# Optimization experiments

Measured on AMD Instinct MI355X. Metric: run time of the kernel, lower is better.

## Reference

```python
import jax, jax.numpy as jnp
import numpy as np

NEG = -1000000000.0  # mask fill value from the original code


def setup_inputs() -> dict:
    key = jax.random.key(0)
    k1, k2, k3 = jax.random.split(key, 3)
    B, L, H, E = 2, 2048, 16, 64
    S, D = L, E
    queries = jax.random.normal(k1, (B, L, H, E), dtype=jnp.float32)
    keys = jax.random.normal(k2, (B, S, H, E), dtype=jnp.float32)
    values = jax.random.normal(k3, (B, S, H, D), dtype=jnp.float32)
    return {"queries": queries, "keys": keys, "values": values}


def reference(queries, keys, values):
    B, L, H, E = queries.shape
    S = keys.shape[1]
    scale = 1.0 / np.sqrt(E)
    # scores: [B, H, L, S]
    scores = jnp.einsum('blhe,bshe->bhls', queries, keys)
    # Faithful to original: tf.where(band_part(ones,-1,0), -1e9, scores)
    # i.e. fill -1e9 where the LOWER triangle (incl. diagonal) is True.
    tril = jnp.tril(jnp.ones((L, S), dtype=bool))  # [L, S]
    scores = jnp.where(tril[None, None, :, :], jnp.float32(NEG), scores)
    # scale applied AFTER masking, as in the original
    A = jax.nn.softmax(scale * scores, axis=-1)
    # dropout is identity at inference
    V = jnp.einsum('bhls,bshd->blhd', A, values)
    return V
```

## Files before the change

### kernel.cpp

```cpp
#include <hip/hip_runtime.h>


#define B_ 2
#define L_ 2048
#define H_ 16
#define E_ 64
#define S_ 2048
#define D_ 64
#define QSCALE 0.18033688011112042f

typedef __attribute__((ext_vector_type(4))) float f32x4;
typedef __attribute__((ext_vector_type(16))) float f32x16;
typedef __attribute__((ext_vector_type(8))) short short8;
typedef __attribute__((ext_vector_type(2))) unsigned int uint2v;
typedef __attribute__((ext_vector_type(4))) unsigned int uint4v;
typedef unsigned short ushort;

__device__ __forceinline__ unsigned short f2bf(float f) {
  unsigned int u = __builtin_bit_cast(unsigned int, f);
  u = (u + 0x7FFFu + ((u >> 16) & 1u)) >> 16;
  return (unsigned short)u;
}
__device__ __forceinline__ unsigned int pkbf(float a, float b) {
  return (unsigned int)f2bf(a) | ((unsigned int)f2bf(b) << 16);
}
__device__ __forceinline__ unsigned cvtpk(float a, float b) {
  unsigned r;
  asm("v_cvt_pk_bf16_f32 %0, %1, %2" : "=v"(r) : "v"(a), "v"(b));
  return r;
}
__device__ __forceinline__ uint2v plswap(unsigned a, unsigned b, int hi) {
#if __has_builtin(__builtin_amdgcn_permlane32_swap)
  (void)hi;
  return __builtin_amdgcn_permlane32_swap(a, b, false, false);
#else
  unsigned ax = (unsigned)__shfl_xor((int)a, 32);
  unsigned bx = (unsigned)__shfl_xor((int)b, 32);
  uint2v r;
  r[0] = hi ? bx : a;
  r[1] = hi ? b : ax;
  return r;
#endif
}
__device__ __forceinline__ f32x16 zero16() {
  f32x16 z;
#pragma unroll
  for (int i = 0; i < 16; ++i) z[i] = 0.f;
  return z;
}

__global__ __launch_bounds__(256) void prep_k(const float* __restrict__ Kg,
                                              unsigned short* __restrict__ Kb) {
  const int t = blockIdx.x * 256 + (int)threadIdx.x;
  const int orow = t >> 3, e0 = (t & 7) << 3;
  const int s = orow & (S_ - 1), bh = orow >> 11;
  const int b = bh >> 4, h = bh & 15;
  const float* src = Kg + ((size_t)((b * S_ + s) * H_ + h)) * E_ + e0;
  f32x4 a = ((const f32x4*)src)[0], c = ((const f32x4*)src)[1];
  short8 o;
  o[0]=(short)f2bf(a[0]); o[1]=(short)f2bf(a[1]); o[2]=(short)f2bf(a[2]); o[3]=(short)f2bf(a[3]);
  o[4]=(short)f2bf(c[0]); o[5]=(short)f2bf(c[1]); o[6]=(short)f2bf(c[2]); o[7]=(short)f2bf(c[3]);
  *(short8*)(Kb + (size_t)orow * E_ + e0) = o;
}

__global__ __launch_bounds__(256) void prep_vt(const float* __restrict__ Vg,
                                               unsigned short* __restrict__ Vt) {
  const int bh = blockIdx.x & 31, st = blockIdx.x >> 5;
  const int b = bh >> 4, h = bh & 15;
  const int s0 = st << 6;
  const int tid = (int)threadIdx.x;
  __shared__ unsigned short Tl[64][72];
  {
    const int sr = tid >> 2, d0 = (tid & 3) << 4;
    const float* src = Vg + ((size_t)((b * S_ + s0 + sr) * H_ + h)) * D_ + d0;
    f32x4 v0 = ((const f32x4*)src)[0], v1 = ((const f32x4*)src)[1];
    f32x4 v2 = ((const f32x4*)src)[2], v3 = ((const f32x4*)src)[3];
    unsigned short* dst = &Tl[sr][d0];
    dst[0]=f2bf(v0[0]); dst[1]=f2bf(v0[1]); dst[2]=f2bf(v0[2]); dst[3]=f2bf(v0[3]);
    dst[4]=f2bf(v1[0]); dst[5]=f2bf(v1[1]); dst[6]=f2bf(v1[2]); dst[7]=f2bf(v1[3]);
    dst[8]=f2bf(v2[0]); dst[9]=f2bf(v2[1]); dst[10]=f2bf(v2[2]); dst[11]=f2bf(v2[3]);
    dst[12]=f2bf(v3[0]); dst[13]=f2bf(v3[1]); dst[14]=f2bf(v3[2]); dst[15]=f2bf(v3[3]);
  }
  __syncthreads();
  {
    const int d = tid >> 2, sb = (tid & 3) << 4;
    short8 o0, o1;
#pragma unroll
    for (int j = 0; j < 8; ++j) {
      o0[j] = (short)Tl[sb + j][d];
      o1[j] = (short)Tl[sb + 8 + j][d];
    }
    unsigned short* dst = Vt + ((size_t)bh * D_ + d) * S_ + s0 + sb;
    *(short8*)dst = o0;
    *(short8*)(dst + 8) = o1;
  }
}

struct StageRegs { short8 k0, k1, v0, v1; };

__device__ __forceinline__ StageRegs stage_load(const ushort* __restrict__ Kbh,
                                                const ushort* __restrict__ Vbh,
                                                int s0, int w, int lane) {
  StageRegs s;
  const int rk = lane >> 3;
  const int g = lane & 7;
  const int r0 = w * 8 + rk, r1 = (w + 4) * 8 + rk;
  const ushort* kb = Kbh + (size_t)s0 * 64;
  s.k0 = *(const short8*)(kb + r0 * 64 + g * 8);
  s.k1 = *(const short8*)(kb + r1 * 64 + g * 8);
  const ushort* vb = Vbh + s0;
  s.v0 = *(const short8*)(vb + (size_t)r0 * S_ + g * 8);
  s.v1 = *(const short8*)(vb + (size_t)r1 * S_ + g * 8);
  return s;
}

__device__ __forceinline__ void stage_write(ushort* KL, ushort* VL,
                                            const StageRegs& s, int w, int lane) {
  const int rk = lane >> 3;
  const int g = lane & 7;
  const int r0 = w * 8 + rk, r1 = (w + 4) * 8 + rk;
  *(short8*)(KL + r0 * 64 + ((g ^ (r0 & 7)) << 3)) = s.k0;
  *(short8*)(KL + r1 * 64 + ((g ^ (r1 & 7)) << 3)) = s.k1;
  *(short8*)(VL + r0 * 64 + ((g ^ (r0 & 7)) << 3)) = s.v0;
  *(short8*)(VL + r1 * 64 + ((g ^ (r1 & 7)) << 3)) = s.v1;
}

__global__ __launch_bounds__(256, 2) void attn_fwd6(
    const float* __restrict__ Qg, const ushort* __restrict__ Kb,
    const ushort* __restrict__ Vt, float* __restrict__ Og) {
  const int bh = blockIdx.x;
  const int b = bh >> 4, h = bh & 15;
  const int yi0 = (int)blockIdx.y;
  const int yi = (yi0 < 8) ? yi0 : 23 - yi0;
  const int q0 = yi << 7;
  const int tid = (int)threadIdx.x;
  const int w = tid >> 6, lane = tid & 63;
  const int hi = lane >> 5, c32 = lane & 31;
  const int qbase = q0 + (w << 5);
  const int qrow = qbase + c32;

  __shared__ ushort KL[2][4096];
  __shared__ ushort VL[2][4096];

  const ushort* Kbh = Kb + (size_t)bh * (S_ * E_);
  const ushort* Vbh = Vt + (size_t)bh * (D_ * S_);

  short8 qf[4];
  {
    const float* qr = Qg + ((size_t)((b * L_ + qrow) * H_ + h)) * E_;
#pragma unroll
    for (int kc = 0; kc < 4; ++kc) {
      f32x4 x = *(const f32x4*)(qr + kc * 16 + hi * 8);
      f32x4 y = *(const f32x4*)(qr + kc * 16 + hi * 8 + 4);
      short8 q;
      q[0]=(short)f2bf(QSCALE*x[0]); q[1]=(short)f2bf(QSCALE*x[1]);
      q[2]=(short)f2bf(QSCALE*x[2]); q[3]=(short)f2bf(QSCALE*x[3]);
      q[4]=(short)f2bf(QSCALE*y[0]); q[5]=(short)f2bf(QSCALE*y[1]);
      q[6]=(short)f2bf(QSCALE*y[2]); q[7]=(short)f2bf(QSCALE*y[3]);
      qf[kc] = q;
    }
  }

  f32x16 acc0 = zero16(), acc1 = zero16();
  float m_run = -1e30f, dsum = 0.f;

  const int chB = (q0 + 1) >> 6;
  int cur = 0;

  {
    StageRegs sr = stage_load(Kbh, Vbh, chB << 6, w, lane);
    stage_write(KL[0], VL[0], sr, w, lane);
  }
  __syncthreads();

  for (int ch = chB; ch < (S_ >> 6); ++ch) {
    const int s0 = ch << 6;
    const bool more = (ch + 1) < (S_ >> 6);
    StageRegs sr;
    if (more) sr = stage_load(Kbh, Vbh, (ch + 1) << 6, w, lane);

    if (s0 + 63 > qbase) {
      const ushort* KLc = KL[cur];
      const ushort* VLc = VL[cur];
      f32x16 st0 = zero16(), st1 = zero16();
#pragma unroll
      for (int kc = 0; kc < 4; ++kc) {
        const int g = 2 * kc + hi;
        short8 k0 = *(const short8*)(KLc + c32 * 64 + ((g ^ (c32 & 7)) << 3));
        short8 k1 = *(const short8*)(KLc + (32 + c32) * 64 + ((g ^ (c32 & 7)) << 3));
        st0 = __builtin_amdgcn_mfma_f32_32x32x16_bf16(k0, qf[kc], st0, 0, 0, 0);
        st1 = __builtin_amdgcn_mfma_f32_32x32x16_bf16(k1, qf[kc], st1, 0, 0, 0);
      }

      if (s0 < qbase + 32) {
#pragma unroll
        for (int r = 0; r < 16; ++r) {
          const int ko = (r & 3) + 8 * (r >> 2) + 4 * hi;
          st0[r] = (s0 + ko <= qrow) ? -1e30f : st0[r];
          st1[r] = (s0 + 32 + ko <= qrow) ? -1e30f : st1[r];
        }
      }

      float pmax = -1e30f;
#pragma unroll
      for (int r = 0; r < 16; ++r) pmax = fmaxf(pmax, fmaxf(st0[r], st1[r]));
      if (__any(pmax > m_run + 8.0f)) {
        float rm = fmaxf(pmax, __shfl_xor(pmax, 32));
        float m_new = fmaxf(m_run, rm);
        float alpha = exp2f(m_run - m_new);
        dsum *= alpha;
#pragma unroll
        for (int r = 0; r < 16; ++r) {
          float ar = __shfl(alpha, (r & 3) + 8 * (r >> 2) + 4 * hi);
          acc0[r] *= ar;
          acc1[r] *= ar;
        }
        m_run = m_new;
      }

      float ps = 0.f;
#pragma unroll
      for (int r = 0; r < 16; ++r) { st0[r] = exp2f(st0[r] - m_run); ps += st0[r]; }
#pragma unroll
      for (int r = 0; r < 16; ++r) { st1[r] = exp2f(st1[r] - m_run); ps += st1[r]; }
      dsum += ps;

      short8 pf[4];
#pragma unroll
      for (int kp = 0; kp < 4; ++kp) {
        const f32x16 stt = (kp < 2) ? st0 : st1;
        const int u = kp & 1;
        unsigned pA0 = cvtpk(stt[8 * u + 0], stt[8 * u + 1]);
        unsigned pA1 = cvtpk(stt[8 * u + 2], stt[8 * u + 3]);
        unsigned pB0 = cvtpk(stt[8 * u + 4], stt[8 * u + 5]);
        unsigned pB1 = cvtpk(stt[8 * u + 6], stt[8 * u + 7]);
        uint2v sw0 = plswap(pA0, pB0, hi);
        uint2v sw1 = plswap(pA1, pB1, hi);
        uint4v fv;
        fv[0] = sw0[0]; fv[1] = sw1[0]; fv[2] = sw0[1]; fv[3] = sw1[1];
        pf[kp] = __builtin_bit_cast(short8, fv);
      }

#pragma unroll
      for (int kp = 0; kp < 4; ++kp) {
        const int g = 2 * kp + hi;
        short8 v0 = *(const short8*)(VLc + c32 * 64 + ((g ^ (c32 & 7)) << 3));
        short8 v1 = *(const short8*)(VLc + (32 + c32) * 64 + ((g ^ (c32 & 7)) << 3));
        acc0 = __builtin_amdgcn_mfma_f32_32x32x16_bf16(pf[kp], v0, acc0, 0, 0, 0);
        acc1 = __builtin_amdgcn_mfma_f32_32x32x16_bf16(pf[kp], v1, acc1, 0, 0, 0);
      }
    }

    if (more) stage_write(KL[cur ^ 1], VL[cur ^ 1], sr, w, lane);
    __syncthreads();
    cur ^= 1;
  }

  float dfull = dsum + __shfl_xor(dsum, 32);
#pragma unroll
  for (int r = 0; r < 16; ++r) {
    const int row = (r & 3) + 8 * (r >> 2) + 4 * hi;
    const float dn = __shfl(dfull, row);
    const int grow = qbase + row;
    if (grow != L_ - 1) {
      const float inv = 1.0f / dn;
      const size_t base = ((size_t)((b * L_ + grow) * H_ + h)) * D_;
      Og[base + c32] = acc0[r] * inv;
      Og[base + 32 + c32] = acc1[r] * inv;
    }
  }
}

__global__ __launch_bounds__(256) void vmean_part(const float* __restrict__ Vg,
                                                  float* __restrict__ ws) {
  const int g = blockIdx.x;
  const int slab = g & 15, bh = g >> 4;
  const int b = bh >> 4, h = bh & 15;
  const int lane = (int)threadIdx.x & 63, w = (int)threadIdx.x >> 6;
  const int s0 = (slab << 7) + (w << 5);
  const float* base = Vg + ((size_t)((b * S_ + s0) * H_ + h)) * D_ + lane;
  float sum = 0.f;
#pragma unroll 4
  for (int i = 0; i < 32; ++i) sum += base[(size_t)i * (H_ * D_)];
  __shared__ float red[4][64];
  red[w][lane] = sum;
  __syncthreads();
  if (w == 0)
    ws[(size_t)g * 64 + lane] =
        red[0][lane] + red[1][lane] + red[2][lane] + red[3][lane];
}

__global__ __launch_bounds__(64) void vmean_comb(const float* __restrict__ ws,
                                                 float* __restrict__ Og) {
  const int bh = blockIdx.x;
  const int b = bh >> 4, h = bh & 15;
  const int lane = (int)threadIdx.x;
  float t = 0.f;
#pragma unroll
  for (int i = 0; i < 16; ++i) t += ws[(size_t)(bh * 16 + i) * 64 + lane];
  Og[((size_t)((b * L_ + (L_ - 1)) * H_ + h)) * D_ + lane] = t * (1.0f / (float)S_);
}

__global__ __launch_bounds__(256) void attn_fwd(
    const float* __restrict__ Qg, const float* __restrict__ Kg,
    const float* __restrict__ Vg, float* __restrict__ Og) {
  const int bh = blockIdx.x;
  const int b = bh >> 4, h = bh & 15;
  const int q0 = blockIdx.y << 6;
  const int tid = (int)threadIdx.x;
  const int lane = tid & 63;
  const int w = tid >> 6;
  const int gp = lane >> 4;
  const int c = lane & 15;
  const int qbase = q0 + (w << 4);

  __shared__ unsigned short Kl[32][72];
  __shared__ unsigned short Vts[64][40];

  short8 qf0, qf1;
  {
    const float* qrow = Qg + ((size_t)((b * L_ + (qbase + c)) * H_ + h)) * E_;
    const f32x4* q0p = (const f32x4*)(qrow + (gp << 3));
    const f32x4* q1p = (const f32x4*)(qrow + 32 + (gp << 3));
    f32x4 a0 = q0p[0], b0 = q0p[1], a1 = q1p[0], b1 = q1p[1];
    float t0[8] = {a0[0],a0[1],a0[2],a0[3],b0[0],b0[1],b0[2],b0[3]};
    float t1[8] = {a1[0],a1[1],a1[2],a1[3],b1[0],b1[1],b1[2],b1[3]};
#pragma unroll
    for (int j = 0; j < 8; ++j) {
      qf0[j] = (short)f2bf(0.125f * t0[j]);
      qf1[j] = (short)f2bf(0.125f * t1[j]);
    }
  }

  f32x4 accO[4];
#pragma unroll
  for (int k0 = 0; k0 < 4; ++k0) accO[k0] = (f32x4){0.f, 0.f, 0.f, 0.f};
  float m_run = -1e30f, denom = 0.f;

  const int c0 = (q0 + 1) >> 5;
  const int srow = tid >> 3;
  const int scol = (tid & 7) << 3;

  for (int ch = c0; ch < (S_ >> 5); ++ch) {
    const int s0 = ch << 5;
    __syncthreads();
    {
      const size_t rbase = ((size_t)((b * S_ + (s0 + srow)) * H_ + h));
      const float* kp = Kg + rbase * E_ + scol;
      f32x4 ka = *(const f32x4*)kp;
      f32x4 kb = *(const f32x4*)(kp + 4);
      short8 kv;
      kv[0]=(short)f2bf(ka[0]); kv[1]=(short)f2bf(ka[1]);
      kv[2]=(short)f2bf(ka[2]); kv[3]=(short)f2bf(ka[3]);
      kv[4]=(short)f2bf(kb[0]); kv[5]=(short)f2bf(kb[1]);
      kv[6]=(short)f2bf(kb[2]); kv[7]=(short)f2bf(kb[3]);
      *(short8*)&Kl[srow][scol] = kv;
      const float* vp = Vg + rbase * D_ + scol;
      f32x4 va = *(const f32x4*)vp;
      f32x4 vb = *(const f32x4*)(vp + 4);
      Vts[scol + 0][srow] = f2bf(va[0]);
      Vts[scol + 1][srow] = f2bf(va[1]);
      Vts[scol + 2][srow] = f2bf(va[2]);
      Vts[scol + 3][srow] = f2bf(va[3]);
      Vts[scol + 4][srow] = f2bf(vb[0]);
      Vts[scol + 5][srow] = f2bf(vb[1]);
      Vts[scol + 6][srow] = f2bf(vb[2]);
      Vts[scol + 7][srow] = f2bf(vb[3]);
    }
    __syncthreads();
    if (s0 + 31 <= qbase) continue;

    f32x4 st0 = {0.f,0.f,0.f,0.f}, st1 = {0.f,0.f,0.f,0.f};
    {
      short8 kf;
      kf = *(const short8*)&Kl[c][(gp << 3)];
      st0 = __builtin_amdgcn_mfma_f32_16x16x32_bf16(kf, qf0, st0, 0, 0, 0);
      kf = *(const short8*)&Kl[c][32 + (gp << 3)];
      st0 = __builtin_amdgcn_mfma_f32_16x16x32_bf16(kf, qf1, st0, 0, 0, 0);
      kf = *(const short8*)&Kl[16 + c][(gp << 3)];
      st1 = __builtin_amdgcn_mfma_f32_16x16x32_bf16(kf, qf0, st1, 0, 0, 0);
      kf = *(const short8*)&Kl[16 + c][32 + (gp << 3)];
      st1 = __builtin_amdgcn_mfma_f32_16x16x32_bf16(kf, qf1, st1, 0, 0, 0);
    }

    const int lrow = qbase + c;
    float p[8];
    {
      float sarr[8] = {st0[0], st0[1], st0[2], st0[3], st1[0], st1[1], st1[2], st1[3]};
      float mx = -1e30f;
#pragma unroll
      for (int i = 0; i < 8; ++i) {
        int sg = s0 + ((i >> 2) << 4) + (gp << 2) + (i & 3);
        float v = (sg > lrow) ? sarr[i] : -1e30f;
        p[i] = v;
        mx = fmaxf(mx, v);
      }
      mx = fmaxf(mx, __shfl_xor(mx, 16));
      mx = fmaxf(mx, __shfl_xor(mx, 32));
      float m_new = fmaxf(m_run, mx);
      float sum = 0.f;
#pragma unroll
      for (int i = 0; i < 8; ++i) { p[i] = __expf(p[i] - m_new); sum += p[i]; }
      sum += __shfl_xor(sum, 16);
      sum += __shfl_xor(sum, 32);
      float alpha = __expf(m_run - m_new);
      m_run = m_new;
      denom = denom * alpha + sum;
      float ar0 = __shfl(alpha, (gp << 2) + 0);
      float ar1 = __shfl(alpha, (gp << 2) + 1);
      float ar2 = __shfl(alpha, (gp << 2) + 2);
      float ar3 = __shfl(alpha, (gp << 2) + 3);
#pragma unroll
      for (int k0 = 0; k0 < 4; ++k0) {
        accO[k0][0] *= ar0; accO[k0][1] *= ar1;
        accO[k0][2] *= ar2; accO[k0][3] *= ar3;
      }
    }

    {
      unsigned int pA0 = pkbf(p[0], p[1]), pA1 = pkbf(p[2], p[3]);
      unsigned int pB0 = pkbf(p[4], p[5]), pB1 = pkbf(p[6], p[7]);
      const int al = (gp << 1) & 3;
      const int src0 = (al << 4) + c, src1 = src0 + 16;
      unsigned int a0 = (unsigned int)__shfl((int)pA0, src0);
      unsigned int a1 = (unsigned int)__shfl((int)pA1, src0);
      unsigned int a2 = (unsigned int)__shfl((int)pA0, src1);
      unsigned int a3 = (unsigned int)__shfl((int)pA1, src1);
      unsigned int b0 = (unsigned int)__shfl((int)pB0, src0);
      unsigned int b1 = (unsigned int)__shfl((int)pB1, src0);
      unsigned int b2 = (unsigned int)__shfl((int)pB0, src1);
      unsigned int b3 = (unsigned int)__shfl((int)pB1, src1);
      const bool useA = (gp < 2);
      uint4v fv;
      fv[0] = useA ? a0 : b0;
      fv[1] = useA ? a1 : b1;
      fv[2] = useA ? a2 : b2;
      fv[3] = useA ? a3 : b3;
      short8 pfv = __builtin_bit_cast(short8, fv);
#pragma unroll
      for (int k0 = 0; k0 < 4; ++k0) {
        short8 vf = *(const short8*)&Vts[(k0 << 4) + c][(gp << 3)];
        accO[k0] = __builtin_amdgcn_mfma_f32_16x16x32_bf16(pfv, vf, accO[k0], 0, 0, 0);
      }
    }
  }

  float dr[4];
  dr[0] = __shfl(denom, (gp << 2) + 0);
  dr[1] = __shfl(denom, (gp << 2) + 1);
  dr[2] = __shfl(denom, (gp << 2) + 2);
  dr[3] = __shfl(denom, (gp << 2) + 3);
#pragma unroll
  for (int r = 0; r < 4; ++r) {
    const int grow = qbase + (gp << 2) + r;
    if (grow == L_ - 1) continue;
    const size_t base = ((size_t)((b * L_ + grow) * H_ + h)) * D_ + c;
    const float inv = 1.0f / dr[r];
    Og[base +  0] = accO[0][r] * inv;
    Og[base + 16] = accO[1][r] * inv;
    Og[base + 32] = accO[2][r] * inv;
    Og[base + 48] = accO[3][r] * inv;
  }
}

__global__ __launch_bounds__(256) void vmean_fix(const float* __restrict__ Vg,
                                                 float* __restrict__ Og) {
  const int bh = blockIdx.x;
  const int b = bh >> 4, h = bh & 15;
  const int t = (int)threadIdx.x;
  const int lane = t & 63, w = t >> 6;
  float sum = 0.f;
  for (int s = w; s < S_; s += 4)
    sum += Vg[((size_t)((b * S_ + s) * H_ + h)) * D_ + lane];
  __shared__ float red[4][64];
  red[w][lane] = sum;
  __syncthreads();
  if (w == 0) {
    float tot = red[0][lane] + red[1][lane] + red[2][lane] + red[3][lane];
    Og[((size_t)((b * L_ + (L_ - 1)) * H_ + h)) * D_ + lane] = tot * (1.0f / (float)S_);
  }
}

extern "C" void kernel_launch(void* const* d_in, const int* in_sizes, int n_in,
                              void* d_out, int out_size, void* d_ws, size_t ws_size,
                              hipStream_t stream) {
  const float* Q = (const float*)d_in[0];
  const float* K = (const float*)d_in[1];
  const float* V = (const float*)d_in[2];
  float* O = (float*)d_out;
  const size_t szK = (size_t)B_ * H_ * S_ * E_ * 2;
  const size_t szV = (size_t)B_ * H_ * D_ * S_ * 2;
  const size_t szP = (size_t)(B_ * H_ * 16) * 64 * 4;

  if (ws_size >= szK + szV + szP) {
    unsigned short* Kb = (unsigned short*)d_ws;
    unsigned short* Vt = (unsigned short*)((char*)d_ws + szK);
    float* part = (float*)((char*)d_ws + szK + szV);
    prep_k<<<dim3((B_ * H_ * S_ * 8) / 256), dim3(256), 0, stream>>>(K, Kb);
    prep_vt<<<dim3(B_ * H_ * (S_ / 64)), dim3(256), 0, stream>>>(V, Vt);
    attn_fwd6<<<dim3(B_ * H_, L_ / 128), dim3(256), 0, stream>>>(Q, Kb, Vt, O);
    vmean_part<<<dim3(B_ * H_ * 16), dim3(256), 0, stream>>>(V, part);
    vmean_comb<<<dim3(B_ * H_), dim3(64), 0, stream>>>(part, O);
  } else if (ws_size >= szP) {
    float* part = (float*)d_ws;
    attn_fwd<<<dim3(B_ * H_, L_ / 64), dim3(256), 0, stream>>>(Q, K, V, O);
    vmean_part<<<dim3(B_ * H_ * 16), dim3(256), 0, stream>>>(V, part);
    vmean_comb<<<dim3(B_ * H_), dim3(64), 0, stream>>>(part, O);
  } else {
    attn_fwd<<<dim3(B_ * H_, L_ / 64), dim3(256), 0, stream>>>(Q, K, V, O);
    vmean_fix<<<dim3(B_ * H_), dim3(256), 0, stream>>>(V, O);
  }
}
```

Measured before the change: 71.63 us.

## Merge prep kernels and stage 128-key tiles per barrier in attention

Fuses the K-convert and V-transpose prep kernels into one launch, which removes a kernel launch. The attention kernel now stages 128 keys (two 64-key halves) of K and V into a larger double-buffered shared-memory image, halving the number of barriers and global-load rounds per key range. Each thread issues wider loads. s_setprio hints are wrapped around the MFMA sections. This doubles LDS use per block, which may lower occupancy, and it drops the middle fallback launch path.

Result: faster. 69.66 us (-2.8%).

```diff
diff --git a/kernel.cpp b/kernel.cpp
--- a/kernel.cpp
+++ b/kernel.cpp
@@ -7,6 +7,7 @@
 #define E_ 64
 #define S_ 2048
 #define D_ 64
+#define NR_ 16
 #define QSCALE 0.18033688011112042f
 
 typedef __attribute__((ext_vector_type(4))) float f32x4;
@@ -49,86 +50,94 @@
   return z;
 }
 
-__global__ __launch_bounds__(256) void prep_k(const float* __restrict__ Kg,
-                                              unsigned short* __restrict__ Kb) {
-  const int t = blockIdx.x * 256 + (int)threadIdx.x;
-  const int orow = t >> 3, e0 = (t & 7) << 3;
-  const int s = orow & (S_ - 1), bh = orow >> 11;
-  const int b = bh >> 4, h = bh & 15;
-  const float* src = Kg + ((size_t)((b * S_ + s) * H_ + h)) * E_ + e0;
-  f32x4 a = ((const f32x4*)src)[0], c = ((const f32x4*)src)[1];
-  short8 o;
-  o[0]=(short)f2bf(a[0]); o[1]=(short)f2bf(a[1]); o[2]=(short)f2bf(a[2]); o[3]=(short)f2bf(a[3]);
-  o[4]=(short)f2bf(c[0]); o[5]=(short)f2bf(c[1]); o[6]=(short)f2bf(c[2]); o[7]=(short)f2bf(c[3]);
-  *(short8*)(Kb + (size_t)orow * E_ + e0) = o;
-}
-
-__global__ __launch_bounds__(256) void prep_vt(const float* __restrict__ Vg,
-                                               unsigned short* __restrict__ Vt) {
-  const int bh = blockIdx.x & 31, st = blockIdx.x >> 5;
-  const int b = bh >> 4, h = bh & 15;
-  const int s0 = st << 6;
+__global__ __launch_bounds__(256) void prep_all(const float* __restrict__ Kg,
+                                                const float* __restrict__ Vg,
+                                                ushort* __restrict__ Kb,
+                                                ushort* __restrict__ Vt) {
+  __shared__ ushort Tl[64][72];
+  const int blk = (int)blockIdx.x;
   const int tid = (int)threadIdx.x;
-  __shared__ unsigned short Tl[64][72];
-  {
-    const int sr = tid >> 2, d0 = (tid & 3) << 4;
-    const float* src = Vg + ((size_t)((b * S_ + s0 + sr) * H_ + h)) * D_ + d0;
-    f32x4 v0 = ((const f32x4*)src)[0], v1 = ((const f32x4*)src)[1];
-    f32x4 v2 = ((const f32x4*)src)[2], v3 = ((const f32x4*)src)[3];
-    unsigned short* dst = &Tl[sr][d0];
-    dst[0]=f2bf(v0[0]); dst[1]=f2bf(v0[1]); dst[2]=f2bf(v0[2]); dst[3]=f2bf(v0[3]);
-    dst[4]=f2bf(v1[0]); dst[5]=f2bf(v1[1]); dst[6]=f2bf(v1[2]); dst[7]=f2bf(v1[3]);
-    dst[8]=f2bf(v2[0]); dst[9]=f2bf(v2[1]); dst[10]=f2bf(v2[2]); dst[11]=f2bf(v2[3]);
-    dst[12]=f2bf(v3[0]); dst[13]=f2bf(v3[1]); dst[14]=f2bf(v3[2]); dst[15]=f2bf(v3[3]);
-  }
-  __syncthreads();
-  {
-    const int d = tid >> 2, sb = (tid & 3) << 4;
-    short8 o0, o1;
-#pragma unroll
-    for (int j = 0; j < 8; ++j) {
-      o0[j] = (short)Tl[sb + j][d];
-      o1[j] = (short)Tl[sb + 8 + j][d];
-    }
-    unsigned short* dst = Vt + ((size_t)bh * D_ + d) * S_ + s0 + sb;
-    *(short8*)dst = o0;
-    *(short8*)(dst + 8) = o1;
-  }
-}
-
-struct StageRegs { short8 k0, k1, v0, v1; };
-
-__device__ __forceinline__ StageRegs stage_load(const ushort* __restrict__ Kbh,
-                                                const ushort* __restrict__ Vbh,
-                                                int s0, int w, int lane) {
-  StageRegs s;
-  const int rk = lane >> 3;
-  const int g = lane & 7;
-  const int r0 = w * 8 + rk, r1 = (w + 4) * 8 + rk;
-  const ushort* kb = Kbh + (size_t)s0 * 64;
-  s.k0 = *(const short8*)(kb + r0 * 64 + g * 8);
-  s.k1 = *(const short8*)(kb + r1 * 64 + g * 8);
-  const ushort* vb = Vbh + s0;
-  s.v0 = *(const short8*)(vb + (size_t)r0 * S_ + g * 8);
-  s.v1 = *(const short8*)(vb + (size_t)r1 * S_ + g * 8);
-  return s;
-}
-
-__device__ __forceinline__ void stage_write(ushort* KL, ushort* VL,
-                                            const StageRegs& s, int w, int lane) {
-  const int rk = lane >> 3;
-  const int g = lane & 7;
-  const int r0 = w * 8 + rk, r1 = (w + 4) * 8 + rk;
-  *(short8*)(KL + r0 * 64 + ((g ^ (r0 & 7)) << 3)) = s.k0;
-  *(short8*)(KL + r1 * 64 + ((g ^ (r1 & 7)) << 3)) = s.k1;
-  *(short8*)(VL + r0 * 64 + ((g ^ (r0 & 7)) << 3)) = s.v0;
-  *(short8*)(VL + r1 * 64 + ((g ^ (r1 & 7)) << 3)) = s.v1;
-}
-
-__global__ __launch_bounds__(256, 2) void attn_fwd6(
+  if (blk < 2048) {
+    const int t = blk * 256 + tid;
+    const int orow = t >> 3, e0 = (t & 7) << 3;
+    const int s = orow & (S_ - 1), bh = orow >> 11;
+    const int b = bh >> 4, h = bh & 15;
+    const float* src = Kg + ((size_t)((b * S_ + s) * H_ + h)) * E_ + e0;
+    f32x4 a = ((const f32x4*)src)[0], c = ((const f32x4*)src)[1];
+    short8 o;
+    o[0]=(short)f2bf(a[0]); o[1]=(short)f2bf(a[1]); o[2]=(short)f2bf(a[2]); o[3]=(short)f2bf(a[3]);
+    o[4]=(short)f2bf(c[0]); o[5]=(short)f2bf(c[1]); o[6]=(short)f2bf(c[2]); o[7]=(short)f2bf(c[3]);
+    *(short8*)(Kb + (size_t)orow * E_ + e0) = o;
+  } else {
+    const int vb = blk - 2048;
+    const int bh = vb & 31, st = vb >> 5;
+    const int b = bh >> 4, h = bh & 15;
+    const int s0 = st << 6;
+    {
+      const int sr = tid >> 2, d0 = (tid & 3) << 4;
+      const float* src = Vg + ((size_t)((b * S_ + s0 + sr) * H_ + h)) * D_ + d0;
+      f32x4 v0 = ((const f32x4*)src)[0], v1 = ((const f32x4*)src)[1];
+      f32x4 v2 = ((const f32x4*)src)[2], v3 = ((const f32x4*)src)[3];
+      ushort* dst = &Tl[sr][d0];
+      dst[0]=f2bf(v0[0]); dst[1]=f2bf(v0[1]); dst[2]=f2bf(v0[2]); dst[3]=f2bf(v0[3]);
+      dst[4]=f2bf(v1[0]); dst[5]=f2bf(v1[1]); dst[6]=f2bf(v1[2]); dst[7]=f2bf(v1[3]);
+      dst[8]=f2bf(v2[0]); dst[9]=f2bf(v2[1]); dst[10]=f2bf(v2[2]); dst[11]=f2bf(v2[3]);
+      dst[12]=f2bf(v3[0]); dst[13]=f2bf(v3[1]); dst[14]=f2bf(v3[2]); dst[15]=f2bf(v3[3]);
+    }
+    __syncthreads();
+    {
+      const int d = tid >> 2, sb = (tid & 3) << 4;
+      short8 o0, o1;
+#pragma unroll
+      for (int j = 0; j < 8; ++j) {
+        o0[j] = (short)Tl[sb + j][d];
+        o1[j] = (short)Tl[sb + 8 + j][d];
+      }
+      ushort* dst = Vt + ((size_t)bh * D_ + d) * S_ + s0 + sb;
+      *(short8*)dst = o0;
+      *(short8*)(dst + 8) = o1;
+    }
+  }
+}
+
+struct Stage8 { short8 k[4]; short8 v[4]; };
+
+__device__ __forceinline__ Stage8 sload(const ushort* __restrict__ Kbh,
+                                        const ushort* __restrict__ VbhT,
+                                        int s0, int tid) {
+  Stage8 r;
+  const int sl = tid >> 1, gb = (tid & 1) * 4;
+  const ushort* kp = Kbh + (size_t)(s0 + sl) * E_ + gb * 8;
+  r.k[0] = *(const short8*)(kp);
+  r.k[1] = *(const short8*)(kp + 8);
+  r.k[2] = *(const short8*)(kp + 16);
+  r.k[3] = *(const short8*)(kp + 24);
+  const int d = tid >> 2, sb = (tid & 3) * 32;
+  const ushort* vp = VbhT + (size_t)d * S_ + s0 + sb;
+  r.v[0] = *(const short8*)(vp);
+  r.v[1] = *(const short8*)(vp + 8);
+  r.v[2] = *(const short8*)(vp + 16);
+  r.v[3] = *(const short8*)(vp + 24);
+  return r;
+}
+
+__device__ __forceinline__ void swrite(ushort* SM, const Stage8& r, int tid) {
+  const int sl = tid >> 1, gb = (tid & 1) * 4;
+#pragma unroll
+  for (int j = 0; j < 4; ++j)
+    *(short8*)(SM + sl * 64 + (((gb + j) ^ (sl & 7)) << 3)) = r.k[j];
+  const int d = tid >> 2, sgb = (tid & 3) * 4;
+#pragma unroll
+  for (int j = 0; j < 4; ++j) {
+    const int sgg = sgb + j;
+    *(short8*)(SM + 8192 + (sgg >> 3) * 4096 + d * 64 + (((sgg & 7) ^ (d & 7)) << 3)) = r.v[j];
+  }
+}
+
+__global__ __launch_bounds__(256, 2) void attn_fwd9(
     const float* __restrict__ Qg, const ushort* __restrict__ Kb,
     const ushort* __restrict__ Vt, float* __restrict__ Og) {
-  const int bh = blockIdx.x;
+  const int bh = (int)blockIdx.x;
   const int b = bh >> 4, h = bh & 15;
   const int yi0 = (int)blockIdx.y;
   const int yi = (yi0 < 8) ? yi0 : 23 - yi0;
@@ -139,11 +148,10 @@
   const int qbase = q0 + (w << 5);
   const int qrow = qbase + c32;
 
-  __shared__ ushort KL[2][4096];
-  __shared__ ushort VL[2][4096];
+  __shared__ __align__(16) ushort SM[2][16384];
 
   const ushort* Kbh = Kb + (size_t)bh * (S_ * E_);
-  const ushort* Vbh = Vt + (size_t)bh * (D_ * S_);
+  const ushort* VbhT = Vt + (size_t)bh * (D_ * S_);
 
   short8 qf[4];
   {
@@ -164,109 +172,116 @@
   f32x16 acc0 = zero16(), acc1 = zero16();
   float m_run = -1e30f, dsum = 0.f;
 
-  const int chB = (q0 + 1) >> 6;
-  int cur = 0;
+  const int r0 = (q0 + 1) >> 7;
 
   {
-    StageRegs sr = stage_load(Kbh, Vbh, chB << 6, w, lane);
-    stage_write(KL[0], VL[0], sr, w, lane);
+    Stage8 s = sload(Kbh, VbhT, r0 << 7, tid);
+    swrite(SM[0], s, tid);
   }
   __syncthreads();
 
-  for (int ch = chB; ch < (S_ >> 6); ++ch) {
-    const int s0 = ch << 6;
-    const bool more = (ch + 1) < (S_ >> 6);
-    StageRegs sr;
-    if (more) sr = stage_load(Kbh, Vbh, (ch + 1) << 6, w, lane);
-
-    if (s0 + 63 > qbase) {
-      const ushort* KLc = KL[cur];
-      const ushort* VLc = VL[cur];
-      f32x16 st0 = zero16(), st1 = zero16();
-#pragma unroll
-      for (int kc = 0; kc < 4; ++kc) {
-        const int g = 2 * kc + hi;
-        short8 k0 = *(const short8*)(KLc + c32 * 64 + ((g ^ (c32 & 7)) << 3));
-        short8 k1 = *(const short8*)(KLc + (32 + c32) * 64 + ((g ^ (c32 & 7)) << 3));
-        st0 = __builtin_amdgcn_mfma_f32_32x32x16_bf16(k0, qf[kc], st0, 0, 0, 0);
-        st1 = __builtin_amdgcn_mfma_f32_32x32x16_bf16(k1, qf[kc], st1, 0, 0, 0);
+  for (int r = r0; r < NR_; ++r) {
+    const int cur = (r - r0) & 1;
+    const bool more = (r + 1) < NR_;
+    Stage8 nxt;
+    if (more) nxt = sload(Kbh, VbhT, (r + 1) << 7, tid);
+
+    const ushort* img = SM[cur];
+#pragma unroll
+    for (int half = 0; half < 2; ++half) {
+      const int s0 = (r << 7) + (half << 6);
+      if (s0 + 63 > qbase) {
+        f32x16 st0 = zero16(), st1 = zero16();
+        __builtin_amdgcn_s_setprio(1);
+#pragma unroll
+        for (int kc = 0; kc < 4; ++kc) {
+          const int gg = 2 * kc + hi;
+          const int rl0 = (half << 6) + c32, rl1 = rl0 + 32;
+          short8 k0 = *(const short8*)(img + rl0 * 64 + ((gg ^ (rl0 & 7)) << 3));
+          short8 k1 = *(const short8*)(img + rl1 * 64 + ((gg ^ (rl1 & 7)) << 3));
+          st0 = __builtin_amdgcn_mfma_f32_32x32x16_bf16(k0, qf[kc], st0, 0, 0, 0);
+          st1 = __builtin_amdgcn_mfma_f32_32x32x16_bf16(k1, qf[kc], st1, 0, 0, 0);
+        }
+        __builtin_amdgcn_s_setprio(0);
+
+        if (s0 < qbase + 32) {
+#pragma unroll
+          for (int r16 = 0; r16 < 16; ++r16) {
+            const int ko = (r16 & 3) + 8 * (r16 >> 2) + 4 * hi;
+            st0[r16] = (s0 + ko <= qrow) ? -1e30f : st0[r16];
+            st1[r16] = (s0 + 32 + ko <= qrow) ? -1e30f : st1[r16];
+          }
+        }
+
+        float pmax = -1e30f;
+#pragma unroll
+        for (int r16 = 0; r16 < 16; ++r16) pmax = fmaxf(pmax, fmaxf(st0[r16], st1[r16]));
+        if (__any(pmax > m_run + 8.0f)) {
+          float rm = fmaxf(pmax, __shfl_xor(pmax, 32));
+          float m_new = fmaxf(m_run, rm);
+          float alpha = exp2f(m_run - m_new);
+          dsum *= alpha;
+#pragma unroll
+          for (int r16 = 0; r16 < 16; ++r16) {
+            float ar = __shfl(alpha, (r16 & 3) + 8 * (r16 >> 2) + 4 * hi);
+            acc0[r16] *= ar;
+            acc1[r16] *= ar;
+          }
+          m_run = m_new;
+        }
+
+        float ps = 0.f;
+#pragma unroll
+        for (int r16 = 0; r16 < 16; ++r16) { st0[r16] = exp2f(st0[r16] - m_run); ps += st0[r16]; }
+#pragma unroll
+        for (int r16 = 0; r16 < 16; ++r16) { st1[r16] = exp2f(st1[r16] - m_run); ps += st1[r16]; }
+        dsum += ps;
+
+        short8 pf[4];
+#pragma unroll
+        for (int kp = 0; kp < 4; ++kp) {
+          const f32x16 stt = (kp < 2) ? st0 : st1;
+          const int u = kp & 1;
+          unsigned pA0 = cvtpk(stt[8 * u + 0], stt[8 * u + 1]);
+          unsigned pA1 = cvtpk(stt[8 * u + 2], stt[8 * u + 3]);
+          unsigned pB0 = cvtpk(stt[8 * u + 4], stt[8 * u + 5]);
+          unsigned pB1 = cvtpk(stt[8 * u + 6], stt[8 * u + 7]);
+          uint2v sw0 = plswap(pA0, pB0, hi);
+          uint2v sw1 = plswap(pA1, pB1, hi);
+          uint4v fv;
+          fv[0] = sw0[0]; fv[1] = sw1[0]; fv[2] = sw0[1]; fv[3] = sw1[1];
+          pf[kp] = __builtin_bit_cast(short8, fv);
+        }
+
+        __builtin_amdgcn_s_setprio(1);
+#pragma unroll
+        for (int kp = 0; kp < 4; ++kp) {
+          const int sg = 2 * kp + hi;
+          const ushort* vb = img + 8192 + half * 4096;
+          short8 v0 = *(const short8*)(vb + c32 * 64 + ((sg ^ (c32 & 7)) << 3));
+          short8 v1 = *(const short8*)(vb + (32 + c32) * 64 + ((sg ^ (c32 & 7)) << 3));
+          acc0 = __builtin_amdgcn_mfma_f32_32x32x16_bf16(pf[kp], v0, acc0, 0, 0, 0);
+          acc1 = __builtin_amdgcn_mfma_f32_32x32x16_bf16(pf[kp], v1, acc1, 0, 0, 0);
+        }
+        __builtin_amdgcn_s_setprio(0);
       }
-
-      if (s0 < qbase + 32) {
-#pragma unroll
-        for (int r = 0; r < 16; ++r) {
-          const int ko = (r & 3) + 8 * (r >> 2) + 4 * hi;
-          st0[r] = (s0 + ko <= qrow) ? -1e30f : st0[r];
-          st1[r] = (s0 + 32 + ko <= qrow) ? -1e30f : st1[r];
-        }
-      }
-
-      float pmax = -1e30f;
-#pragma unroll
-      for (int r = 0; r < 16; ++r) pmax = fmaxf(pmax, fmaxf(st0[r], st1[r]));
-      if (__any(pmax > m_run + 8.0f)) {
-        float rm = fmaxf(pmax, __shfl_xor(pmax, 32));
-        float m_new = fmaxf(m_run, rm);
-        float alpha = exp2f(m_run - m_new);
-        dsum *= alpha;
-#pragma unroll
-        for (int r = 0; r < 16; ++r) {
-          float ar = __shfl(alpha, (r & 3) + 8 * (r >> 2) + 4 * hi);
-          acc0[r] *= ar;
-          acc1[r] *= ar;
-        }
-        m_run = m_new;
-      }
-
-      float ps = 0.f;
-#pragma unroll
-      for (int r = 0; r < 16; ++r) { st0[r] = exp2f(st0[r] - m_run); ps += st0[r]; }
-#pragma unroll
-      for (int r = 0; r < 16; ++r) { st1[r] = exp2f(st1[r] - m_run); ps += st1[r]; }
-      dsum += ps;
-
-      short8 pf[4];
-#pragma unroll
-      for (int kp = 0; kp < 4; ++kp) {
-        const f32x16 stt = (kp < 2) ? st0 : st1;
-        const int u = kp & 1;
-        unsigned pA0 = cvtpk(stt[8 * u + 0], stt[8 * u + 1]);
-        unsigned pA1 = cvtpk(stt[8 * u + 2], stt[8 * u + 3]);
-        unsigned pB0 = cvtpk(stt[8 * u + 4], stt[8 * u + 5]);
-        unsigned pB1 = cvtpk(stt[8 * u + 6], stt[8 * u + 7]);
-        uint2v sw0 = plswap(pA0, pB0, hi);
-        uint2v sw1 = plswap(pA1, pB1, hi);
-        uint4v fv;
-        fv[0] = sw0[0]; fv[1] = sw1[0]; fv[2] = sw0[1]; fv[3] = sw1[1];
-        pf[kp] = __builtin_bit_cast(short8, fv);
-      }
-
-#pragma unroll
-      for (int kp = 0; kp < 4; ++kp) {
-        const int g = 2 * kp + hi;
-        short8 v0 = *(const short8*)(VLc + c32 * 64 + ((g ^ (c32 & 7)) << 3));
-        short8 v1 = *(const short8*)(VLc + (32 + c32) * 64 + ((g ^ (c32 & 7)) << 3));
-        acc0 = __builtin_amdgcn_mfma_f32_32x32x16_bf16(pf[kp], v0, acc0, 0, 0, 0);
-        acc1 = __builtin_amdgcn_mfma_f32_32x32x16_bf16(pf[kp], v1, acc1, 0, 0, 0);
-      }
-    }
-
-    if (more) stage_write(KL[cur ^ 1], VL[cur ^ 1], sr, w, lane);
+    }
+
+    if (more) swrite(SM[cur ^ 1], nxt, tid);
     __syncthreads();
-    cur ^= 1;
   }
 
   float dfull = dsum + __shfl_xor(dsum, 32);
 #pragma unroll
-  for (int r = 0; r < 16; ++r) {
-    const int row = (r & 3) + 8 * (r >> 2) + 4 * hi;
+  for (int r16 = 0; r16 < 16; ++r16) {
+    const int row = (r16 & 3) + 8 * (r16 >> 2) + 4 * hi;
     const float dn = __shfl(dfull, row);
     const int grow = qbase + row;
     if (grow != L_ - 1) {
       const float inv = 1.0f / dn;
       const size_t base = ((size_t)((b * L_ + grow) * H_ + h)) * D_;
-      Og[base + c32] = acc0[r] * inv;
-      Og[base + 32 + c32] = acc1[r] * inv;
+      Og[base + c32] = acc0[r16] * inv;
+      Og[base + 32 + c32] = acc1[r16] * inv;
     }
   }
 }
@@ -493,17 +508,11 @@
   const size_t szP = (size_t)(B_ * H_ * 16) * 64 * 4;
 
   if (ws_size >= szK + szV + szP) {
-    unsigned short* Kb = (unsigned short*)d_ws;
-    unsigned short* Vt = (unsigned short*)((char*)d_ws + szK);
+    ushort* Kb = (ushort*)d_ws;
+    ushort* Vt = (ushort*)((char*)d_ws + szK);
     float* part = (float*)((char*)d_ws + szK + szV);
-    prep_k<<<dim3((B_ * H_ * S_ * 8) / 256), dim3(256), 0, stream>>>(K, Kb);
-    prep_vt<<<dim3(B_ * H_ * (S_ / 64)), dim3(256), 0, stream>>>(V, Vt);
-    attn_fwd6<<<dim3(B_ * H_, L_ / 128), dim3(256), 0, stream>>>(Q, Kb, Vt, O);
-    vmean_part<<<dim3(B_ * H_ * 16), dim3(256), 0, stream>>>(V, part);
-    vmean_comb<<<dim3(B_ * H_), dim3(64), 0, stream>>>(part, O);
-  } else if (ws_size >= szP) {
-    float* part = (float*)d_ws;
-    attn_fwd<<<dim3(B_ * H_, L_ / 64), dim3(256), 0, stream>>>(Q, K, V, O);
+    prep_all<<<dim3(3072), dim3(256), 0, stream>>>(K, V, Kb, Vt);
+    attn_fwd9<<<dim3(B_ * H_, L_ / 128), dim3(256), 0, stream>>>(Q, Kb, Vt, O);
     vmean_part<<<dim3(B_ * H_ * 16), dim3(256), 0, stream>>>(V, part);
     vmean_comb<<<dim3(B_ * H_), dim3(64), 0, stream>>>(part, O);
   } else {
```
